# Kernel tuning notes

Measured on AMD Instinct MI355X. Metric: run time of the kernel, lower is better.

The kernel has to match this reference:

```python
import jax, jax.numpy as jnp
import numpy as np

NUM_CLASSES = 133            # thing + stuff classes (void excluded)
NUM_MASK_SLOTS = 128
NUM_GT = 64
NUM_VALID_GT = 48            # remaining gt masks are padded (-1)
ALPHA = 0.75                 # focal_loss_alpha
EPS = 1e-5                   # denominator_epsilon in _mask_similarity
NEG = -999.0                 # _MATCHING_NEGATIVE_CONSTANT
THING_STUFF_IDS = np.arange(NUM_CLASSES, dtype=np.int32)


def setup_inputs() -> dict:
    key = jax.random.key(0)
    k1, k2, k3, k4 = jax.random.split(key, 4)
    B, HW = 8, 161 * 161
    pixel_space_mask_logits = jax.random.normal(k1, (B, HW, NUM_MASK_SLOTS), jnp.float32)
    transformer_class_logits = jax.random.normal(k2, (B, NUM_MASK_SLOTS, NUM_CLASSES + 1), jnp.float32)
    gt_assignment = jax.random.randint(k3, (B, HW), 0, NUM_GT).astype(jnp.int32)
    sem = jax.random.randint(k4, (B, NUM_GT), 0, NUM_CLASSES)
    valid = jnp.arange(NUM_GT) < NUM_VALID_GT
    mask_gt_semantic_map = jnp.where(valid[None, :], sem, -1).astype(jnp.int32)
    return {
        'pixel_space_mask_logits': pixel_space_mask_logits,
        'transformer_class_logits': transformer_class_logits,
        'gt_assignment': gt_assignment,
        'mask_gt_semantic_map': mask_gt_semantic_map,
    }


def _dice_similarity(gt_mask, pred_mask):
    # gt_mask: [B,HW,G] binary, pred_mask: [B,HW,M] softmax -> [B,G,M]
    inter = jnp.einsum('bpg,bpm->bgm', gt_mask, pred_mask)
    denom = (jnp.sum(gt_mask, axis=1)[:, :, None] + jnp.sum(pred_mask, axis=1)[:, None, :]) / 2
    return inter / (denom + EPS)


def _hungarian_min(cost):
    # O(n^3) Kuhn-Munkres with potentials; cost: [n,n] float64. Returns col for each row.
    n = cost.shape[0]
    INF = 1e18
    u = np.zeros(n + 1)
    v = np.zeros(n + 1)
    p = np.zeros(n + 1, dtype=np.int64)
    way = np.zeros(n + 1, dtype=np.int64)
    for i in range(1, n + 1):
        p[0] = i
        j0 = 0
        minv = np.full(n + 1, INF)
        used = np.zeros(n + 1, dtype=bool)
        while True:
            used[j0] = True
            i0 = p[j0]
            cur = cost[i0 - 1, :] - u[i0] - v[1:]
            free = ~used[1:]
            upd = free & (cur < minv[1:])
            minv[1:][upd] = cur[upd]
            way[1:][upd] = j0
            cand = np.where(free, minv[1:], INF)
            j1 = int(np.argmin(cand)) + 1
            delta = cand[j1 - 1]
            u[p[used]] += delta
            v[used] -= delta
            minv[1:][free] -= delta
            j0 = j1
            if p[j0] == 0:
                break
        while j0:
            j1 = way[j0]
            p[j0] = p[j1]
            j0 = j1
    row_for_col = p[1:]
    col_for_row = np.empty(n, dtype=np.int64)
    col_for_row[row_for_col - 1] = np.arange(n)
    return col_for_row


def _nonsquare_hungarian_max(similarity):
    # similarity: [B,G,M] jax array (higher is better). Pads to square with NEG
    # (equivalent to nonsquare_hungarian_matching) and maximizes.
    sim = np.asarray(jax.lax.stop_gradient(similarity), dtype=np.float64)
    B, G, M = sim.shape
    n = max(G, M)
    padded = np.full((B, n, n), NEG, dtype=np.float64)
    padded[:, :G, :M] = sim
    matched = np.stack([_hungarian_min(-padded[b]) for b in range(B)])  # [B,n]
    return jnp.asarray(matched[:, :G], dtype=jnp.int32)  # slot per gt mask


def _forward(pixel_space_mask_logits, transformer_class_logits,
             gt_assignment, mask_gt_semantic_map, matched_slots):
    B, HW, M = pixel_space_mask_logits.shape
    G = mask_gt_semantic_map.shape[1]
    C = transformer_class_logits.shape[-1] - 1  # last channel is void
    gt_mask = jax.nn.one_hot(gt_assignment, G, dtype=jnp.float32)           # [B,HW,G]
    pred_mask = jax.nn.softmax(pixel_space_mask_logits, axis=-1)            # [B,HW,M]
    dice = _dice_similarity(gt_mask, pred_mask)                              # [B,G,M]
    class_prob = jax.nn.softmax(transformer_class_logits, axis=-1)          # [B,M,C+1]
    log_probs = jax.nn.log_softmax(transformer_class_logits, axis=-1)
    valid = (mask_gt_semantic_map >= 0)                                      # [B,G]
    sem_safe = jnp.maximum(mask_gt_semantic_map, 0)
    sem_onehot = jax.nn.one_hot(sem_safe, C + 1, dtype=jnp.float32)          # [B,G,C+1]
    cls_sim = jnp.einsum('bgc,bmc->bgm', sem_onehot, class_prob)             # [B,G,M]

    b_idx = jnp.arange(B)[:, None]
    matched_dice = jnp.take_along_axis(dice, matched_slots[:, :, None], axis=2)[..., 0]     # [B,G]
    matched_cls = jnp.take_along_axis(cls_sim, matched_slots[:, :, None], axis=2)[..., 0]   # [B,G]

    # _generate_mask_slot_semantic_one_hot: scatter-add then gather thing/stuff ids.
    table_width = int(THING_STUFF_IDS.max()) + 2
    full = jnp.zeros((B, M, table_width), jnp.float32)
    full = full.at[b_idx, matched_slots, mask_gt_semantic_map + 1].add(1.0)
    slot_onehot = full[:, :, jnp.asarray(THING_STUFF_IDS) + 1]               # [B,M,C]

    # PQ-style loss. Class term: alpha * dice-weighted CE for matched slots,
    # (1-alpha) * void CE for unmatched slots.
    dice_per_slot = jnp.zeros((B, M), jnp.float32).at[b_idx, matched_slots].add(
        jnp.where(valid, jax.lax.stop_gradient(matched_dice), 0.0))
    pos_ce = -jnp.sum(slot_onehot * log_probs[..., :C], axis=-1)             # [B,M]
    is_pos = jnp.sum(slot_onehot, axis=-1)                                   # 0/1 per slot
    neg_ce = -log_probs[..., C]
    class_loss = jnp.sum(ALPHA * dice_per_slot * pos_ce
                         + (1.0 - ALPHA) * (1.0 - is_pos) * neg_ce) / (B * M)

    # Mask dice term: class-prob-weighted -log dice over valid gt masks.
    dice_loss = jnp.sum(jnp.where(
        valid, -jax.lax.stop_gradient(matched_cls) * jnp.log(matched_dice + EPS), 0.0))
    dice_loss = dice_loss / (jnp.sum(valid.astype(jnp.float32)) + 1.0)

    return class_loss + dice_loss


def reference(pixel_space_mask_logits, transformer_class_logits,
              gt_assignment, mask_gt_semantic_map):
    # Matching similarity = class similarity * mask dice similarity; invalid
    # (padded) gt rows get _MATCHING_NEGATIVE_CONSTANT so they match padding.
    gt_mask = jax.nn.one_hot(gt_assignment, mask_gt_semantic_map.shape[1], dtype=jnp.float32)
    pred_mask = jax.nn.softmax(pixel_space_mask_logits, axis=-1)
    dice = _dice_similarity(gt_mask, pred_mask)
    class_prob = jax.nn.softmax(transformer_class_logits, axis=-1)
    C = transformer_class_logits.shape[-1] - 1
    sem_onehot = jax.nn.one_hot(jnp.maximum(mask_gt_semantic_map, 0), C + 1, dtype=jnp.float32)
    cls_sim = jnp.einsum('bgc,bmc->bgm', sem_onehot, class_prob)
    valid = (mask_gt_semantic_map >= 0)
    similarity = jnp.where(valid[:, :, None], cls_sim * dice, NEG)
    matched_slots = _nonsquare_hungarian_max(similarity)
    return _forward(pixel_space_mask_logits, transformer_class_logits,
                    gt_assignment, mask_gt_semantic_map, matched_slots)
```

## Files before the change

### kernel.cpp

```cpp
#include <hip/hip_runtime.h>
#include <math.h>

#define B_    8
#define HW_   25921
#define M_    128
#define G_    64
#define CP1_  134
#define CLS_  133
#define ALPHA_ 0.75f
#define EPS_   1e-5f

__global__ __launch_bounds__(1024) void kH_bucket(
    const int* __restrict__ gt, int* __restrict__ ordered,
    int* __restrict__ baseg)
{
  __shared__ int cnt[4][G_];
  __shared__ int off[G_];
  const int tid = threadIdx.x;
  const int b = blockIdx.x;
  const int lane = tid & 63, wave = tid >> 6;
  const int* gtb = gt + (size_t)b * HW_;

  for (int i = tid; i < 4 * G_; i += 1024) ((int*)cnt)[i] = 0;
  __syncthreads();
  for (int i = tid; i < HW_; i += 1024)
    atomicAdd(&cnt[tid & 3][gtb[i]], 1);
  __syncthreads();

  if (wave == 0) {
    const int c = cnt[0][lane] + cnt[1][lane] + cnt[2][lane] + cnt[3][lane];
    int inc = c;
    #pragma unroll
    for (int o = 1; o < 64; o <<= 1) {
      const int n = __shfl_up(inc, o);
      if (lane >= o) inc += n;
    }
    const int ex = inc - c;
    off[lane] = ex;
    baseg[b * (G_ + 1) + lane] = ex;
    if (lane == 63) baseg[b * (G_ + 1) + G_] = ex + c;
  }
  __syncthreads();

  int* ob = ordered + (size_t)b * HW_;
  for (int i = tid; i < HW_; i += 1024) {
    const int g = gtb[i];
    const int pos = atomicAdd(&off[g], 1);
    ob[pos] = i;
  }
}

__global__ __launch_bounds__(1024) void kS_gather(
    const float* __restrict__ logits, const int* __restrict__ ordered,
    const int* __restrict__ baseg, float* __restrict__ inter)
{
  __shared__ float red[16][130];
  const int tid = threadIdx.x;
  const int g = blockIdx.x & 63;
  const int b = blockIdx.x >> 6;
  const int lane = tid & 63, wave = tid >> 6;

  const int s0 = baseg[b * (G_ + 1) + g];
  const int s1 = baseg[b * (G_ + 1) + g + 1];
  const int* lst = ordered + (size_t)b * HW_;
  const float* Lb = logits + (size_t)b * HW_ * M_;

  float accx = 0.f, accy = 0.f;
  for (int i = s0 + wave * 8; i < s1; i += 128) {
    bool act[8]; float2 v[8];
    #pragma unroll
    for (int q = 0; q < 8; ++q) {
      act[q] = (i + q) < s1;
      const int idx = lst[act[q] ? (i + q) : (s1 - 1)];
      v[q] = ((const float2*)(Lb + (size_t)idx * M_))[lane];
    }
    float e0[8], e1[8], s[8];
    #pragma unroll
    for (int q = 0; q < 8; ++q) {
      e0[q] = __expf(v[q].x); e1[q] = __expf(v[q].y);
      s[q] = e0[q] + e1[q];
    }
    #pragma unroll
    for (int o = 32; o; o >>= 1) {
      #pragma unroll
      for (int q = 0; q < 8; ++q) s[q] += __shfl_xor(s[q], o);
    }
    #pragma unroll
    for (int q = 0; q < 8; ++q) {
      if (act[q]) {
        const float inv = 1.0f / s[q];
        accx += e0[q] * inv;
        accy += e1[q] * inv;
      }
    }
  }
  red[wave][2 * lane]     = accx;
  red[wave][2 * lane + 1] = accy;
  __syncthreads();
  if (tid < M_) {
    float s = 0.f;
    #pragma unroll
    for (int w = 0; w < 16; ++w) s += red[w][tid];
    inter[((size_t)b * G_ + g) * M_ + tid] = s;
  }
}

#define ISTR 130
#define CSTR 129

__device__ __forceinline__ double embed_idx(double a, int idx) {
  long long bl = __double_as_longlong(a);
  bl = (bl & ~0xFFll) | (long long)idx;
  return __longlong_as_double(bl);
}

__global__ __launch_bounds__(1024) void k4_match_loss(
    const float* __restrict__ inter, const float* __restrict__ cl,
    const int* __restrict__ semmap, float* __restrict__ out)
{
  __shared__ float interL[G_ * ISTR];
  __shared__ float expSL[48 * CSTR];
  __shared__ float costL[48 * CSTR];
  __shared__ float lseL[M_], negceL[M_], sumpredL[M_], cntL[G_];
  __shared__ int   semL[G_], validg[G_];
  __shared__ int   ivA[M_], prowA[M_], colofL[G_];
  __shared__ int   nvL, nvtotL;

  const int tid = threadIdx.x;
  const int b = blockIdx.x;
  const int lane = tid & 63, wave = tid >> 6;

  if (tid < G_) semL[tid] = semmap[b * G_ + tid];
  for (int i = tid; i < G_ * M_; i += 1024) {
    const int g = i >> 7, m = i & 127;
    interL[g * ISTR + m] = inter[(size_t)b * G_ * M_ + i];
  }
  for (int r = wave; r < M_; r += 16) {
    const float* x = cl + ((size_t)b * M_ + r) * CP1_;
    float a = x[lane];
    float bb = (lane + 64  < CP1_) ? x[lane + 64]  : -1e30f;
    float cc = (lane + 128 < CP1_) ? x[lane + 128] : -1e30f;
    float mx = fmaxf(a, fmaxf(bb, cc));
    #pragma unroll
    for (int o = 32; o; o >>= 1) mx = fmaxf(mx, __shfl_xor(mx, o));
    float s = __expf(a - mx);
    if (lane + 64  < CP1_) s += __expf(bb - mx);
    if (lane + 128 < CP1_) s += __expf(cc - mx);
    #pragma unroll
    for (int o = 32; o; o >>= 1) s += __shfl_xor(s, o);
    const float lse = mx + logf(s);
    if (lane == 0) lseL[r] = lse;
    if (lane == CLS_ - 128) negceL[r] = lse - cc;
  }
  __syncthreads();

  if (wave == 0) {
    const int sv = semL[tid];
    const unsigned long long vm = __ballot(sv >= 0);
    if (sv >= 0) {
      const int rank = __popcll(vm & ((1ull << tid) - 1ull));
      validg[rank] = tid;
    }
    if (tid == 0) nvL = (int)__popcll(vm);
    int c = 0;
    #pragma unroll
    for (int kk = 0; kk < (B_ * G_) / 64; ++kk)
      c += (semmap[tid + 64 * kk] >= 0) ? 1 : 0;
    #pragma unroll
    for (int o = 32; o; o >>= 1) c += __shfl_xor(c, o);
    if (tid == 0) nvtotL = c;
  }
  __syncthreads();
  const int nv = min(nvL, 48);

  if (tid < M_) {
    float s = 0.f;
    for (int g = 0; g < G_; ++g) s += interL[g * ISTR + tid];
    sumpredL[tid] = s;
  } else if (tid < M_ + G_) {
    const int g = tid - M_;
    float s = 0.f;
    for (int m = 0; m < M_; ++m) s += interL[g * ISTR + m];
    cntL[g] = s;
  } else if (tid >= 256) {
    for (int i = tid - 256; i < nv * M_; i += 768) {
      const int r = i >> 7, m = i & 127;
      const int sem = semL[validg[r]];
      expSL[r * CSTR + m] =
        __expf(cl[((size_t)b * M_ + m) * CP1_ + sem] - lseL[m]);
    }
  }
  __syncthreads();

  for (int i = tid; i < nv * M_; i += 1024) {
    const int r = i >> 7, m = i & 127;
    const int g = validg[r];
    const float dice = interL[g * ISTR + m] /
                       ((cntL[g] + sumpredL[m]) * 0.5f + EPS_);
    costL[r * CSTR + m] = -(expSL[r * CSTR + m] * dice);
  }
  __syncthreads();

  if (wave != 0) return;
  const int t = tid;

  double u_reg = 0.0;
  if (t < nv) {
    float bv = 1e30f;
    for (int m = 0; m < M_; ++m) {
      const float c = costL[t * CSTR + m];
      if (c < bv) bv = c;
    }
    u_reg = (double)bv;
  }
  double v0d = 0.0, v1d = 0.0;
  {
    double m0 = 1e18, m1 = 1e18; int i0 = 0, i1 = 0;
    for (int i = 0; i < nv; ++i) {
      const double ui = __shfl(u_reg, i);
      const double c0 = (double)costL[i * CSTR + t] - ui;
      const double c1 = (double)costL[i * CSTR + t + 64] - ui;
      if (c0 < m0) { m0 = c0; i0 = i; }
      if (c1 < m1) { m1 = c1; i1 = i; }
    }
    v0d = m0; v1d = m1;
    ivA[t] = i0; ivA[t + 64] = i1;
  }
  prowA[t] = 0; prowA[t + 64] = 0;
  if (t < G_) colofL[t] = -1;
  if (t == 0) {
    unsigned long long rowfree = (nv < 64) ? ((1ull << nv) - 1ull) : ~0ull;
    for (int j = 0; j < M_; ++j) {
      const int r = ivA[j];
      if ((rowfree >> r) & 1ull) {
        rowfree &= ~(1ull << r);
        prowA[j] = r + 1;
        colofL[r] = j;
      }
    }
  }
  unsigned long long um = __ballot(t < nv && colofL[t] < 0);

  int way0, way1;
  while (um) {
    const int iRow = (int)__builtin_ctzll(um) + 1;
    um &= um - 1;
    double minv0 = 1e18, minv1 = 1e18;
    bool used0 = false, used1 = false;
    bool inTree = false;
    way0 = 0; way1 = 0;
    int j0 = 0, i0 = iRow;
    for (int guard = 0; guard < 2 * M_ + 4; ++guard) {
      if (j0 != 0) {
        const int src = (j0 - 1) & 63, hi = (j0 - 1) >> 6;
        if (t == src) { if (hi) used1 = true; else used0 = true; }
      }
      if (t == i0 - 1) inTree = true;
      const double ui0 = __shfl(u_reg, i0 - 1);
      const float c0 = costL[(i0 - 1) * CSTR + t];
      const float c1 = costL[(i0 - 1) * CSTR + t + 64];
      if (!used0) { const double cur = (double)c0 - ui0 - v0d; if (cur < minv0) { minv0 = cur; way0 = j0; } }
      if (!used1) { const double cur = (double)c1 - ui0 - v1d; if (cur < minv1) { minv1 = cur; way1 = j0; } }
      const double a0 = used0 ? 1e18 : minv0;
      const double a1 = used1 ? 1e18 : minv1;
      double pk = fmin(embed_idx(a0, t + 1), embed_idx(a1, t + 65));
      #pragma unroll
      for (int o = 32; o; o >>= 1) pk = fmin(pk, __shfl_xor(pk, o));
      const int j1 = (int)(__double_as_longlong(pk) & 0xFF);
      const int src1 = (j1 - 1) & 63, hi1 = (j1 - 1) >> 6;
      const double d0s = __shfl(minv0, src1);
      const double d1s = __shfl(minv1, src1);
      const double delta = hi1 ? d1s : d0s;
      const int pr = prowA[j1 - 1];
      if (used0) v0d -= delta; else minv0 -= delta;
      if (used1) v1d -= delta; else minv1 -= delta;
      if (inTree) u_reg += delta;
      j0 = j1;
      if (pr == 0) break;
      i0 = pr;
    }
    int j = j0;
    for (int guard = 0; guard <= M_ && j; ++guard) {
      const int src = (j - 1) & 63, hi = (j - 1) >> 6;
      const int wl = __shfl(way0, src), wh = __shfl(way1, src);
      const int jp = hi ? wh : wl;
      const int newr = (jp == 0) ? iRow : prowA[jp - 1];
      if (t == 0) prowA[j - 1] = newr;
      j = jp;
    }
  }

  double clsum = 0.0, dsum = 0.0;
  #pragma unroll
  for (int h = 0; h < 2; ++h) {
    const int m = t + 64 * h;
    const int pr = prowA[m];
    const float* lpbm = cl + ((size_t)b * M_ + m) * CP1_;
    if (pr > 0) {
      const int r = pr - 1;
      const int g = validg[r];
      const float md = interL[g * ISTR + m] /
                       ((cntL[g] + sumpredL[m]) * 0.5f + EPS_);
      const float lpx = lpbm[semL[g]] - lseL[m];
      const float es = expSL[r * CSTR + m];
      clsum += (double)(ALPHA_ * md * (-lpx));
      dsum  += (double)(-es * logf(md + EPS_));
    } else {
      clsum += (double)((1.0f - ALPHA_) * negceL[m]);
    }
  }
  #pragma unroll
  for (int o = 32; o; o >>= 1) {
    clsum += __shfl_xor(clsum, o);
    dsum  += __shfl_xor(dsum, o);
  }
  if (t == 0) {
    const float contrib = (float)(clsum / (double)(B_ * M_) +
                                  dsum / (double)(nvtotL + 1));
    atomicAdd(out, contrib);
  }
}

extern "C" void kernel_launch(void* const* d_in, const int* in_sizes, int n_in,
                              void* d_out, int out_size, void* d_ws, size_t ws_size,
                              hipStream_t stream) {
  const float* logits = (const float*)d_in[0];
  const float* cl     = (const float*)d_in[1];
  const int*   gt     = (const int*)d_in[2];
  const int*   semmap = (const int*)d_in[3];
  float* out = (float*)d_out;

  int*   ordered = (int*)d_ws;
  int*   baseg   = ordered + (size_t)B_ * HW_;
  float* inter   = (float*)(baseg + B_ * (G_ + 1));

  hipMemsetAsync(d_out, 0, sizeof(float), stream);
  hipLaunchKernelGGL(kH_bucket, dim3(B_), dim3(1024), 0, stream,
                     gt, ordered, baseg);
  hipLaunchKernelGGL(kS_gather, dim3(B_ * G_), dim3(1024), 0, stream,
                     logits, ordered, baseg, inter);
  hipLaunchKernelGGL(k4_match_loss, dim3(B_), dim3(1024), 0, stream,
                     inter, cl, semmap, out);
}
```

Baseline: 226.2 us.

## Parallelize bucketing into count/prefix/scatter and split gather per group

Replaces the single-block-per-batch bucketing kernel with a three-stage count, prefix and scatter pipeline over 16 chunks per batch, so 128 blocks work instead of 8. The gather kernel now uses two 512-thread blocks per (batch, group), each covering half the group's pixel list, and stages the index list in shared memory. The two partial intersection sums are added when loaded in the matching kernel. This adds two extra kernel launches and doubles the intermediate buffer, in exchange for filling more compute units during the histogram and gather phases.

```diff
diff --git a/kernel.cpp b/kernel.cpp
--- a/kernel.cpp
+++ b/kernel.cpp
@@ -9,86 +9,118 @@
 #define CLS_  133
 #define ALPHA_ 0.75f
 #define EPS_   1e-5f
-
-__global__ __launch_bounds__(1024) void kH_bucket(
-    const int* __restrict__ gt, int* __restrict__ ordered,
-    int* __restrict__ baseg)
+#define NCH_  16
+#define CHSZ_ 1621
+#define LCAP_ 640
+
+__global__ __launch_bounds__(256) void kH1_count(
+    const int* __restrict__ gt, int* __restrict__ cnts)
 {
   __shared__ int cnt[4][G_];
+  const int tid = threadIdx.x;
+  const int b = blockIdx.x >> 4, c = blockIdx.x & 15;
+  const int p0 = c * CHSZ_, p1 = min(p0 + CHSZ_, HW_);
+  const int* gtb = gt + (size_t)b * HW_;
+  for (int i = tid; i < 4 * G_; i += 256) ((int*)cnt)[i] = 0;
+  __syncthreads();
+  for (int p = p0 + tid; p < p1; p += 256)
+    atomicAdd(&cnt[tid & 3][gtb[p]], 1);
+  __syncthreads();
+  if (tid < G_)
+    cnts[(blockIdx.x << 6) + tid] =
+      cnt[0][tid] + cnt[1][tid] + cnt[2][tid] + cnt[3][tid];
+}
+
+__global__ __launch_bounds__(512) void kH2_prefix(
+    const int* __restrict__ cnts, int* __restrict__ baseg)
+{
+  const int b = threadIdx.x >> 6, g = threadIdx.x & 63;
+  int tot = 0;
+  #pragma unroll
+  for (int c = 0; c < NCH_; ++c) tot += cnts[((b * NCH_ + c) << 6) + g];
+  int inc = tot;
+  #pragma unroll
+  for (int o = 1; o < 64; o <<= 1) {
+    const int n = __shfl_up(inc, o);
+    if (g >= o) inc += n;
+  }
+  const int ex = inc - tot;
+  baseg[b * (G_ + 1) + g] = ex;
+  if (g == 63) baseg[b * (G_ + 1) + G_] = ex + tot;
+}
+
+__global__ __launch_bounds__(256) void kH3_scatter(
+    const int* __restrict__ gt, const int* __restrict__ cnts,
+    const int* __restrict__ baseg, int* __restrict__ ordered)
+{
   __shared__ int off[G_];
   const int tid = threadIdx.x;
-  const int b = blockIdx.x;
-  const int lane = tid & 63, wave = tid >> 6;
+  const int b = blockIdx.x >> 4, c = blockIdx.x & 15;
+  const int p0 = c * CHSZ_, p1 = min(p0 + CHSZ_, HW_);
   const int* gtb = gt + (size_t)b * HW_;
-
-  for (int i = tid; i < 4 * G_; i += 1024) ((int*)cnt)[i] = 0;
-  __syncthreads();
-  for (int i = tid; i < HW_; i += 1024)
-    atomicAdd(&cnt[tid & 3][gtb[i]], 1);
-  __syncthreads();
-
-  if (wave == 0) {
-    const int c = cnt[0][lane] + cnt[1][lane] + cnt[2][lane] + cnt[3][lane];
-    int inc = c;
-    #pragma unroll
-    for (int o = 1; o < 64; o <<= 1) {
-      const int n = __shfl_up(inc, o);
-      if (lane >= o) inc += n;
-    }
-    const int ex = inc - c;
-    off[lane] = ex;
-    baseg[b * (G_ + 1) + lane] = ex;
-    if (lane == 63) baseg[b * (G_ + 1) + G_] = ex + c;
-  }
-  __syncthreads();
-
+  if (tid < G_) {
+    int o = baseg[b * (G_ + 1) + tid];
+    for (int cp = 0; cp < c; ++cp) o += cnts[((b * NCH_ + cp) << 6) + tid];
+    off[tid] = o;
+  }
+  __syncthreads();
   int* ob = ordered + (size_t)b * HW_;
-  for (int i = tid; i < HW_; i += 1024) {
-    const int g = gtb[i];
-    const int pos = atomicAdd(&off[g], 1);
-    ob[pos] = i;
-  }
-}
-
-__global__ __launch_bounds__(1024) void kS_gather(
+  for (int p = p0 + tid; p < p1; p += 256) {
+    const int pos = atomicAdd(&off[gtb[p]], 1);
+    ob[pos] = p;
+  }
+}
+
+__global__ __launch_bounds__(512) void kS_gather(
     const float* __restrict__ logits, const int* __restrict__ ordered,
-    const int* __restrict__ baseg, float* __restrict__ inter)
-{
-  __shared__ float red[16][130];
+    const int* __restrict__ baseg, float* __restrict__ interP)
+{
+  __shared__ float red[8][130];
+  __shared__ int   lstL[LCAP_];
   const int tid = threadIdx.x;
-  const int g = blockIdx.x & 63;
-  const int b = blockIdx.x >> 6;
+  const int s = blockIdx.x & 1;
+  const int g = (blockIdx.x >> 1) & 63;
+  const int b = blockIdx.x >> 7;
   const int lane = tid & 63, wave = tid >> 6;
 
   const int s0 = baseg[b * (G_ + 1) + g];
   const int s1 = baseg[b * (G_ + 1) + g + 1];
-  const int* lst = ordered + (size_t)b * HW_;
+  const int n = s1 - s0;
+  const int half = (n + 1) >> 1;
+  const int start = s0 + s * half;
+  const int end = min(start + half, s1);
+  const int cnt = end - start;
+  const int* lst = ordered + (size_t)b * HW_ + start;
   const float* Lb = logits + (size_t)b * HW_ * M_;
 
+  for (int i = tid; i < cnt && i < LCAP_; i += 512) lstL[i] = lst[i];
+  __syncthreads();
+
   float accx = 0.f, accy = 0.f;
-  for (int i = s0 + wave * 8; i < s1; i += 128) {
+  for (int i = wave * 8; i < cnt; i += 64) {
     bool act[8]; float2 v[8];
     #pragma unroll
     for (int q = 0; q < 8; ++q) {
-      act[q] = (i + q) < s1;
-      const int idx = lst[act[q] ? (i + q) : (s1 - 1)];
+      act[q] = (i + q) < cnt;
+      const int li = act[q] ? (i + q) : (cnt - 1);
+      const int idx = (li < LCAP_) ? lstL[li] : lst[li];
       v[q] = ((const float2*)(Lb + (size_t)idx * M_))[lane];
     }
-    float e0[8], e1[8], s[8];
+    float e0[8], e1[8], sm[8];
     #pragma unroll
     for (int q = 0; q < 8; ++q) {
       e0[q] = __expf(v[q].x); e1[q] = __expf(v[q].y);
-      s[q] = e0[q] + e1[q];
+      sm[q] = e0[q] + e1[q];
     }
     #pragma unroll
     for (int o = 32; o; o >>= 1) {
       #pragma unroll
-      for (int q = 0; q < 8; ++q) s[q] += __shfl_xor(s[q], o);
+      for (int q = 0; q < 8; ++q) sm[q] += __shfl_xor(sm[q], o);
     }
     #pragma unroll
     for (int q = 0; q < 8; ++q) {
       if (act[q]) {
-        const float inv = 1.0f / s[q];
+        const float inv = 1.0f / sm[q];
         accx += e0[q] * inv;
         accy += e1[q] * inv;
       }
@@ -98,10 +130,10 @@
   red[wave][2 * lane + 1] = accy;
   __syncthreads();
   if (tid < M_) {
-    float s = 0.f;
-    #pragma unroll
-    for (int w = 0; w < 16; ++w) s += red[w][tid];
-    inter[((size_t)b * G_ + g) * M_ + tid] = s;
+    float sv = 0.f;
+    #pragma unroll
+    for (int w = 0; w < 8; ++w) sv += red[w][tid];
+    interP[(((size_t)b * 2 + s) * G_ + g) * M_ + tid] = sv;
   }
 }
 
@@ -115,7 +147,7 @@
 }
 
 __global__ __launch_bounds__(1024) void k4_match_loss(
-    const float* __restrict__ inter, const float* __restrict__ cl,
+    const float* __restrict__ interP, const float* __restrict__ cl,
     const int* __restrict__ semmap, float* __restrict__ out)
 {
   __shared__ float interL[G_ * ISTR];
@@ -131,9 +163,13 @@
   const int lane = tid & 63, wave = tid >> 6;
 
   if (tid < G_) semL[tid] = semmap[b * G_ + tid];
-  for (int i = tid; i < G_ * M_; i += 1024) {
-    const int g = i >> 7, m = i & 127;
-    interL[g * ISTR + m] = inter[(size_t)b * G_ * M_ + i];
+  {
+    const float* ip0 = interP + (size_t)(b * 2 + 0) * G_ * M_;
+    const float* ip1 = interP + (size_t)(b * 2 + 1) * G_ * M_;
+    for (int i = tid; i < G_ * M_; i += 1024) {
+      const int g = i >> 7, m = i & 127;
+      interL[g * ISTR + m] = ip0[i] + ip1[i];
+    }
   }
   for (int r = wave; r < M_; r += 16) {
     const float* x = cl + ((size_t)b * M_ + r) * CP1_;
@@ -330,15 +366,20 @@
   const int*   semmap = (const int*)d_in[3];
   float* out = (float*)d_out;
 
-  int*   ordered = (int*)d_ws;
-  int*   baseg   = ordered + (size_t)B_ * HW_;
-  float* inter   = (float*)(baseg + B_ * (G_ + 1));
+  int*   cnts    = (int*)d_ws;
+  int*   baseg   = cnts + B_ * NCH_ * G_;
+  int*   ordered = baseg + B_ * (G_ + 1);
+  float* interP  = (float*)(ordered + (size_t)B_ * HW_);
 
   hipMemsetAsync(d_out, 0, sizeof(float), stream);
-  hipLaunchKernelGGL(kH_bucket, dim3(B_), dim3(1024), 0, stream,
-                     gt, ordered, baseg);
-  hipLaunchKernelGGL(kS_gather, dim3(B_ * G_), dim3(1024), 0, stream,
-                     logits, ordered, baseg, inter);
+  hipLaunchKernelGGL(kH1_count, dim3(B_ * NCH_), dim3(256), 0, stream,
+                     gt, cnts);
+  hipLaunchKernelGGL(kH2_prefix, dim3(1), dim3(512), 0, stream,
+                     cnts, baseg);
+  hipLaunchKernelGGL(kH3_scatter, dim3(B_ * NCH_), dim3(256), 0, stream,
+                     gt, cnts, baseg, ordered);
+  hipLaunchKernelGGL(kS_gather, dim3(B_ * G_ * 2), dim3(512), 0, stream,
+                     logits, ordered, baseg, interP);
   hipLaunchKernelGGL(k4_match_loss, dim3(B_), dim3(1024), 0, stream,
-                     inter, cl, semmap, out);
-}
+                     interP, cl, semmap, out);
+}
```

Result: faster. 216.9 us (-4.1%).
